# Performance work log

Hardware: AMD Instinct MI355X
Metric: run time of the kernel (lower is better)

The kernel has to match this reference:

```python
import jax, jax.numpy as jnp
import numpy as np

PAD = 2  # F.conv2d(padding=2) with 5x5 kernels -> SAME

def setup_inputs() -> dict:
    key = jax.random.key(0)
    k1, k2 = jax.random.split(key)
    B, H, W, C = 64, 128, 128, 3
    KH, KW, N = 5, 5, 10  # last_frames(2) * num_transformed_images(5)
    images = jax.random.uniform(k1, (B, H, W, C), dtype=jnp.float32)
    kernels = jax.random.uniform(k2, (B, KH, KW, N), dtype=jnp.float32)
    return {"images": images, "kernels": kernels}


def reference(images, kernels):
    """Faithful JAX version of apply_cdna_kernels.

    images:  [B, H, W, C]
    kernels: [B, KH, KW, N]
    returns: [N, B, C, H, W] (the torch code returns N split tensors of
             shape [1, B, C, H, W]; we return the equivalent stacked array).
    Implemented as a single grouped cross-correlation with
    feature_group_count=B, fusing the per-batch F.conv2d loop.
    """
    B, H, W, C = images.shape
    _, KH, KW, N = kernels.shape
    # torch: images.permute([3,0,1,2]) -> [C, B, H, W]; treat C as conv batch,
    # B as input channels, one input channel per group.
    inp = jnp.transpose(images, (3, 0, 1, 2))  # [C, B, H, W]
    # weights: group b owns output channels b*N:(b+1)*N, each 1 input channel
    w = jnp.transpose(kernels, (0, 3, 1, 2)).reshape(B * N, 1, KH, KW)
    out = jax.lax.conv_general_dilated(
        inp, w,
        window_strides=(1, 1),
        padding=((PAD, PAD), (PAD, PAD)),
        feature_group_count=B,
        dimension_numbers=("NCHW", "OIHW", "NCHW"),
    )  # [C, B*N, H, W]
    out = out.reshape(C, B, N, H, W)
    return jnp.transpose(out, (2, 1, 0, 3, 4))  # [N, B, C, H, W]
```

## Files before the change

kernel.cpp:

```cpp
#include <hip/hip_runtime.h>


#define B_  64
#define H_  128
#define W_  128
#define C_  3
#define N_  10
#define KH_ 5
#define KW_ 5
#define TH_ 8
#define TW_ 32
#define HALO 2
#define LDS_ROW ((TW_ + 2*HALO) * C_)
#define LDS_ELEMS ((TH_ + 2*HALO) * LDS_ROW)

__global__ __launch_bounds__(256, 4) void cdna_apply_kernel(
    const float* __restrict__ images,
    const float* __restrict__ kernels,
    float* __restrict__ out)
{
    __shared__ float s_img[LDS_ELEMS];

    const int tid = threadIdx.x;
    const int bid = blockIdx.x;
    const int b   = bid >> 6;
    const int t   = bid & 63;
    const int by  = t >> 2;
    const int bx  = t & 3;
    const int y0  = by * TH_;
    const int x0  = bx * TW_;

    const long img_base = (long)b * (H_ * W_ * C_);
    #pragma unroll
    for (int i = tid; i < LDS_ELEMS; i += 256) {
        int yy = i / LDS_ROW;
        int r  = i - yy * LDS_ROW;
        int xx = r / C_;
        int c  = r - xx * C_;
        int y  = y0 + yy - HALO;
        int x  = x0 + xx - HALO;
        float v = 0.0f;
        if ((unsigned)y < (unsigned)H_ && (unsigned)x < (unsigned)W_)
            v = images[img_base + (long)y * (W_ * C_) + x * C_ + c];
        s_img[i] = v;
    }
    __syncthreads();

    const int tx = tid & (TW_ - 1);
    const int ty = tid >> 5;

    const float* __restrict__ kb = kernels + b * (KH_ * KW_ * N_);

    float acc[N_ * C_];
    #pragma unroll
    for (int i = 0; i < N_ * C_; ++i) acc[i] = 0.0f;

    #pragma unroll 1
    for (int kh = 0; kh < KH_; ++kh) {
        const float* row = &s_img[(ty + kh) * LDS_ROW + tx * C_];
        float p[KW_ * C_];
        #pragma unroll
        for (int i = 0; i < KW_ * C_; ++i) p[i] = row[i];

        const float* __restrict__ wrow = kb + kh * (KW_ * N_);
        #pragma unroll
        for (int kw = 0; kw < KW_; ++kw) {
            #pragma unroll
            for (int n = 0; n < N_; ++n) {
                const float wgt = wrow[kw * N_ + n];
                acc[n * C_ + 0] = fmaf(p[kw * C_ + 0], wgt, acc[n * C_ + 0]);
                acc[n * C_ + 1] = fmaf(p[kw * C_ + 1], wgt, acc[n * C_ + 1]);
                acc[n * C_ + 2] = fmaf(p[kw * C_ + 2], wgt, acc[n * C_ + 2]);
            }
        }
    }

    const int h = y0 + ty;
    const int w = x0 + tx;
    float* ob = out + (long)b * (C_ * H_ * W_) + (long)h * W_ + w;
    #pragma unroll
    for (int n = 0; n < N_; ++n) {
        #pragma unroll
        for (int c = 0; c < C_; ++c) {
            ob[(long)n * ((long)B_ * C_ * H_ * W_) + (long)c * (H_ * W_)] = acc[n * C_ + c];
        }
    }
}

extern "C" void kernel_launch(void* const* d_in, const int* in_sizes, int n_in,
                              void* d_out, int out_size, void* d_ws, size_t ws_size,
                              hipStream_t stream) {
    const float* images  = (const float*)d_in[0];
    const float* kernels = (const float*)d_in[1];
    float* out = (float*)d_out;

    const int grid = B_ * (H_ / TH_) * (W_ / TW_);
    cdna_apply_kernel<<<grid, 256, 0, stream>>>(images, kernels, out);
}
```

Before: 148.9 us.

## Parallelize over output kernel index with register-blocked 2x4 pixel tiles and vector IO

The grid becomes (N, H/16, B), so each block handles one output kernel over full-width 16-row strips. Each thread computes a 2x4 pixel tile for all three channels, holding its 25 weights in registers and reusing loaded LDS rows across both output rows. Loads use float2/float4 and stores use float4. The cost is that the image tile is reloaded into LDS once per output kernel (10x more input traffic), in exchange for far fewer LDS reads per FMA and coalesced vector stores.

```diff
diff --git a/kernel.cpp b/kernel.cpp
--- a/kernel.cpp
+++ b/kernel.cpp
@@ -8,82 +8,101 @@
 #define N_  10
 #define KH_ 5
 #define KW_ 5
-#define TH_ 8
-#define TW_ 32
-#define HALO 2
-#define LDS_ROW ((TW_ + 2*HALO) * C_)
-#define LDS_ELEMS ((TH_ + 2*HALO) * LDS_ROW)
+#define TH_ 16
+#define LDS_ROWS (TH_ + 4)
+#define ROW_F ((W_ + 4) * C_)
+#define ROW_VALID (W_ * C_)
 
 __global__ __launch_bounds__(256, 4) void cdna_apply_kernel(
     const float* __restrict__ images,
     const float* __restrict__ kernels,
     float* __restrict__ out)
 {
-    __shared__ float s_img[LDS_ELEMS];
+    __shared__ __align__(16) float s_img[LDS_ROWS * ROW_F];
 
     const int tid = threadIdx.x;
-    const int bid = blockIdx.x;
-    const int b   = bid >> 6;
-    const int t   = bid & 63;
-    const int by  = t >> 2;
-    const int bx  = t & 3;
-    const int y0  = by * TH_;
-    const int x0  = bx * TW_;
+    const int n   = blockIdx.x;
+    const int ht  = blockIdx.y;
+    const int b   = blockIdx.z;
+    const int y0  = ht * TH_;
 
-    const long img_base = (long)b * (H_ * W_ * C_);
+    const float* __restrict__ ib = images + (long)b * (H_ * W_ * C_);
+    for (int i = tid; i < LDS_ROWS * (ROW_F / 4); i += 256) {
+        const int r  = i / (ROW_F / 4);
+        const int q  = i - r * (ROW_F / 4);
+        const int y  = y0 + r - 2;
+        float v0 = 0.f, v1 = 0.f, v2 = 0.f, v3 = 0.f;
+        if ((unsigned)y < (unsigned)H_) {
+            const float* grow = ib + (long)y * ROW_VALID;
+            const int f0 = q * 4 - 6;
+            if (f0 >= 0 && f0 <= ROW_VALID - 4) {
+                const float2 a = *(const float2*)(grow + f0);
+                const float2 c2 = *(const float2*)(grow + f0 + 2);
+                v0 = a.x; v1 = a.y; v2 = c2.x; v3 = c2.y;
+            } else {
+                if (f0 + 0 >= 0 && f0 + 0 < ROW_VALID) v0 = grow[f0 + 0];
+                if (f0 + 1 >= 0 && f0 + 1 < ROW_VALID) v1 = grow[f0 + 1];
+                if (f0 + 2 >= 0 && f0 + 2 < ROW_VALID) v2 = grow[f0 + 2];
+                if (f0 + 3 >= 0 && f0 + 3 < ROW_VALID) v3 = grow[f0 + 3];
+            }
+        }
+        *(float4*)(&s_img[r * ROW_F + q * 4]) = make_float4(v0, v1, v2, v3);
+    }
+
+    float wt[KH_ * KW_];
     #pragma unroll
-    for (int i = tid; i < LDS_ELEMS; i += 256) {
-        int yy = i / LDS_ROW;
-        int r  = i - yy * LDS_ROW;
-        int xx = r / C_;
-        int c  = r - xx * C_;
-        int y  = y0 + yy - HALO;
-        int x  = x0 + xx - HALO;
-        float v = 0.0f;
-        if ((unsigned)y < (unsigned)H_ && (unsigned)x < (unsigned)W_)
-            v = images[img_base + (long)y * (W_ * C_) + x * C_ + c];
-        s_img[i] = v;
-    }
+    for (int k = 0; k < KH_ * KW_; ++k)
+        wt[k] = kernels[(long)b * (KH_ * KW_ * N_) + k * N_ + n];
+
     __syncthreads();
 
-    const int tx = tid & (TW_ - 1);
+    const int tx = tid & 31;
     const int ty = tid >> 5;
 
-    const float* __restrict__ kb = kernels + b * (KH_ * KW_ * N_);
+    float acc0[12], acc1[12];
+    #pragma unroll
+    for (int i = 0; i < 12; ++i) { acc0[i] = 0.f; acc1[i] = 0.f; }
 
-    float acc[N_ * C_];
     #pragma unroll
-    for (int i = 0; i < N_ * C_; ++i) acc[i] = 0.0f;
-
-    #pragma unroll 1
-    for (int kh = 0; kh < KH_; ++kh) {
-        const float* row = &s_img[(ty + kh) * LDS_ROW + tx * C_];
-        float p[KW_ * C_];
+    for (int r = 0; r < 6; ++r) {
+        const float4* rp = (const float4*)&s_img[(ty * 2 + r) * ROW_F + tx * 12];
+        float px[24];
         #pragma unroll
-        for (int i = 0; i < KW_ * C_; ++i) p[i] = row[i];
-
-        const float* __restrict__ wrow = kb + kh * (KW_ * N_);
-        #pragma unroll
-        for (int kw = 0; kw < KW_; ++kw) {
+        for (int j = 0; j < 6; ++j) {
+            const float4 t = rp[j];
+            px[j * 4 + 0] = t.x; px[j * 4 + 1] = t.y;
+            px[j * 4 + 2] = t.z; px[j * 4 + 3] = t.w;
+        }
+        if (r < 5) {
             #pragma unroll
-            for (int n = 0; n < N_; ++n) {
-                const float wgt = wrow[kw * N_ + n];
-                acc[n * C_ + 0] = fmaf(p[kw * C_ + 0], wgt, acc[n * C_ + 0]);
-                acc[n * C_ + 1] = fmaf(p[kw * C_ + 1], wgt, acc[n * C_ + 1]);
-                acc[n * C_ + 2] = fmaf(p[kw * C_ + 2], wgt, acc[n * C_ + 2]);
+            for (int kw = 0; kw < KW_; ++kw) {
+                const float wgt = wt[r * KW_ + kw];
+                #pragma unroll
+                for (int w = 0; w < 4; ++w)
+                    #pragma unroll
+                    for (int c = 0; c < C_; ++c)
+                        acc0[c * 4 + w] = fmaf(px[(kw + w) * 3 + c], wgt, acc0[c * 4 + w]);
+            }
+        }
+        if (r >= 1) {
+            #pragma unroll
+            for (int kw = 0; kw < KW_; ++kw) {
+                const float wgt = wt[(r - 1) * KW_ + kw];
+                #pragma unroll
+                for (int w = 0; w < 4; ++w)
+                    #pragma unroll
+                    for (int c = 0; c < C_; ++c)
+                        acc1[c * 4 + w] = fmaf(px[(kw + w) * 3 + c], wgt, acc1[c * 4 + w]);
             }
         }
     }
 
-    const int h = y0 + ty;
-    const int w = x0 + tx;
-    float* ob = out + (long)b * (C_ * H_ * W_) + (long)h * W_ + w;
+    const long HW = (long)H_ * W_;
+    float* ob = out + ((long)n * B_ + b) * (C_ * HW) + (long)(y0 + ty * 2) * W_ + tx * 4;
     #pragma unroll
-    for (int n = 0; n < N_; ++n) {
-        #pragma unroll
-        for (int c = 0; c < C_; ++c) {
-            ob[(long)n * ((long)B_ * C_ * H_ * W_) + (long)c * (H_ * W_)] = acc[n * C_ + c];
-        }
+    for (int c = 0; c < C_; ++c) {
+        *(float4*)(ob + c * HW)      = make_float4(acc0[c*4+0], acc0[c*4+1], acc0[c*4+2], acc0[c*4+3]);
+        *(float4*)(ob + c * HW + W_) = make_float4(acc1[c*4+0], acc1[c*4+1], acc1[c*4+2], acc1[c*4+3]);
     }
 }
 
@@ -94,6 +113,6 @@
     const float* kernels = (const float*)d_in[1];
     float* out = (float*)d_out;
 
-    const int grid = B_ * (H_ / TH_) * (W_ / TW_);
+    dim3 grid(N_, H_ / TH_, B_);
     cdna_apply_kernel<<<grid, 256, 0, stream>>>(images, kernels, out);
 }
```

Result: slower. 204.8 us (+37.6%).
